# Kernel optimization log

Measured on AMD Instinct MI355X. Metric: run time of the kernel, lower is better.

Reference implementation:

```python
import jax, jax.numpy as jnp
import numpy as np

V, A, N, C = 3, 4, 50000, 128


def setup_inputs() -> dict:
    key = jax.random.key(0)
    k1, k2, k3 = jax.random.split(key, 3)
    x = jax.random.normal(k1, (V, A, N, C), dtype=jnp.float32)
    # per-view Linear(in=C, out=C): weight [out,in], bias [out]
    W = jax.random.normal(k2, (V, C, C), dtype=jnp.float32) / np.sqrt(C)
    b = jax.random.normal(k3, (V, C), dtype=jnp.float32) * 0.01
    return {"x": x, "W": W, "b": b}


def reference(x, W, b):
    # per-view linear: out[v,a,n,d] = x[v,a,n,c] @ W[v,d,c]^T + b[v,d]
    out = jnp.einsum('vanc,vdc->vand', x, W) + b[:, None, None, :]
    # view summary: mean over nodes -> [V, A, C]
    s = x.mean(axis=2)
    # attention scores: s . out per node -> [V, A, N]
    scores = jnp.einsum('vac,vanc->van', s, out)
    # tanh then softmax across views (dim 0)
    w = jax.nn.softmax(jnp.tanh(scores), axis=0)
    # weighted combine of views -> [A, N, C]
    return jnp.einsum('van,vanc->anc', w, x)
```

## Files before the change

### kernel.cpp

```cpp
#include <hip/hip_runtime.h>
#include <hip/hip_bf16.h>

#define V 3
#define A 4
#define NN 50000
#define C 128
#define C4 32
#define CHUNKS 128
#define ROWS_PER ((NN + CHUNKS - 1) / CHUNKS)
#define VA (V * A)

__device__ __forceinline__ float dot4(float4 a, float4 b) {
    return a.x * b.x + a.y * b.y + a.z * b.z + a.w * b.w;
}

__device__ __forceinline__ float fast_tanh(float x) {
    float ax = fminf(fabsf(x), 15.f);
    float e  = __expf(2.f * ax);
    float r  = (e - 1.f) * __frcp_rn(e + 1.f);
    return copysignf(r, x);
}

__global__ void k_colsum(const float* __restrict__ x, float* __restrict__ part) {
    const int va    = blockIdx.y;
    const int chunk = blockIdx.x;
    const int n0 = chunk * ROWS_PER;
    const int n1 = (n0 + ROWS_PER < NN) ? (n0 + ROWS_PER) : NN;

    const int lane4 = threadIdx.x & 31;
    const int rowIn = threadIdx.x >> 5;

    const float4* xp = (const float4*)(x + (size_t)va * NN * C);
    float4 acc = {0.f, 0.f, 0.f, 0.f};
    for (int n = n0 + rowIn; n < n1; n += 8) {
        float4 v = xp[(size_t)n * C4 + lane4];
        acc.x += v.x; acc.y += v.y; acc.z += v.z; acc.w += v.w;
    }

    __shared__ float4 red[256];
    red[threadIdx.x] = acc;
    __syncthreads();
    if (threadIdx.x < 32) {
        float4 t = red[threadIdx.x];
        #pragma unroll
        for (int r = 1; r < 8; r++) {
            float4 o = red[threadIdx.x + 32 * r];
            t.x += o.x; t.y += o.y; t.z += o.z; t.w += o.w;
        }
        ((float4*)part)[((size_t)chunk * VA + va) * C4 + lane4] = t;
    }
}

__global__ void k_tvec(const float* __restrict__ part, const float* __restrict__ W,
                       const float* __restrict__ b, float* __restrict__ t,
                       float* __restrict__ c0) {
    const int va = blockIdx.x;
    const int v  = va / A;
    const int c  = threadIdx.x;

    float acc = 0.f;
    #pragma unroll 4
    for (int ch = 0; ch < CHUNKS; ch++)
        acc += part[((size_t)ch * VA + va) * C + c];

    __shared__ float sb[C];
    __shared__ float pb[C];
    sb[c] = acc * (1.0f / (float)NN);
    __syncthreads();

    const float* Wv = W + (size_t)v * C * C;
    float t_acc = 0.f;
    #pragma unroll 8
    for (int d = 0; d < C; d++) t_acc += sb[d] * Wv[d * C + c];
    t[va * C + c] = t_acc;

    pb[c] = sb[c] * b[v * C + c];
    __syncthreads();
    #pragma unroll
    for (int s = 64; s > 0; s >>= 1) {
        if (c < s) pb[c] += pb[c + s];
        __syncthreads();
    }
    if (c == 0) c0[va] = pb[0];
}

__global__ void k_main(const float* __restrict__ x, const float* __restrict__ t,
                       const float* __restrict__ c0, float* __restrict__ out) {
    const int lane = threadIdx.x & 31;
    const int grp  = threadIdx.x >> 5;
    const int a    = blockIdx.y;
    const int n0   = blockIdx.x * 16 + grp * 2;

    const size_t vstride = (size_t)A * NN * C4;
    const float4* xp = (const float4*)x;
    const size_t baseA = ((size_t)a * NN + n0) * C4 + lane;
    const size_t baseB = baseA + C4;

    float4 xa0 = xp[baseA];
    float4 xa1 = xp[baseA + vstride];
    float4 xa2 = xp[baseA + 2 * vstride];
    float4 xb0 = xp[baseB];
    float4 xb1 = xp[baseB + vstride];
    float4 xb2 = xp[baseB + 2 * vstride];

    const float4* tp = (const float4*)t;
    float4 t0 = tp[(0 * A + a) * C4 + lane];
    float4 t1 = tp[(1 * A + a) * C4 + lane];
    float4 t2 = tp[(2 * A + a) * C4 + lane];

    float da0 = dot4(xa0, t0), da1 = dot4(xa1, t1), da2 = dot4(xa2, t2);
    float db0 = dot4(xb0, t0), db1 = dot4(xb1, t1), db2 = dot4(xb2, t2);

    #pragma unroll
    for (int off = 16; off > 0; off >>= 1) {
        da0 += __shfl_xor(da0, off, 32);
        da1 += __shfl_xor(da1, off, 32);
        da2 += __shfl_xor(da2, off, 32);
        db0 += __shfl_xor(db0, off, 32);
        db1 += __shfl_xor(db1, off, 32);
        db2 += __shfl_xor(db2, off, 32);
    }

    const float cc0 = c0[0 * A + a], cc1 = c0[1 * A + a], cc2 = c0[2 * A + a];

    float sa0 = fast_tanh(da0 + cc0);
    float sa1 = fast_tanh(da1 + cc1);
    float sa2 = fast_tanh(da2 + cc2);
    float ma  = fmaxf(sa0, fmaxf(sa1, sa2));
    float ea0 = __expf(sa0 - ma), ea1 = __expf(sa1 - ma), ea2 = __expf(sa2 - ma);
    float inva = __frcp_rn(ea0 + ea1 + ea2);
    float wa0 = ea0 * inva, wa1 = ea1 * inva, wa2 = ea2 * inva;

    float sb0 = fast_tanh(db0 + cc0);
    float sb1 = fast_tanh(db1 + cc1);
    float sb2 = fast_tanh(db2 + cc2);
    float mb  = fmaxf(sb0, fmaxf(sb1, sb2));
    float eb0 = __expf(sb0 - mb), eb1 = __expf(sb1 - mb), eb2 = __expf(sb2 - mb);
    float invb = __frcp_rn(eb0 + eb1 + eb2);
    float wb0 = eb0 * invb, wb1 = eb1 * invb, wb2 = eb2 * invb;

    float4 oa, ob;
    oa.x = wa0 * xa0.x + wa1 * xa1.x + wa2 * xa2.x;
    oa.y = wa0 * xa0.y + wa1 * xa1.y + wa2 * xa2.y;
    oa.z = wa0 * xa0.z + wa1 * xa1.z + wa2 * xa2.z;
    oa.w = wa0 * xa0.w + wa1 * xa1.w + wa2 * xa2.w;
    ob.x = wb0 * xb0.x + wb1 * xb1.x + wb2 * xb2.x;
    ob.y = wb0 * xb0.y + wb1 * xb1.y + wb2 * xb2.y;
    ob.z = wb0 * xb0.z + wb1 * xb1.z + wb2 * xb2.z;
    ob.w = wb0 * xb0.w + wb1 * xb1.w + wb2 * xb2.w;

    float4* op = (float4*)out;
    const size_t obase = ((size_t)a * NN + n0) * C4 + lane;
    op[obase]      = oa;
    op[obase + C4] = ob;
}

extern "C" void kernel_launch(void* const* d_in, const int* in_sizes, int n_in,
                              void* d_out, int out_size, void* d_ws, size_t ws_size,
                              hipStream_t stream) {
    const float* x = (const float*)d_in[0];
    const float* W = (const float*)d_in[1];
    const float* b = (const float*)d_in[2];
    float* out = (float*)d_out;

    float* part = (float*)d_ws;
    float* t    = part + (size_t)CHUNKS * VA * C;
    float* c0   = t + VA * C;

    k_colsum<<<dim3(CHUNKS, VA), 256, 0, stream>>>(x, part);
    k_tvec<<<VA, C, 0, stream>>>(part, W, b, t, c0);
    k_main<<<dim3(NN / 16, A), 256, 0, stream>>>(x, t, c0, out);
}
```

Measured before the change: 506.0 us.

## Reverse main-pass row order, use nontemporal stores, split tvec reduction, unroll colsum

The main kernel now walks rows in reverse, so the rows the column-sum pass touched last are read first and may still sit in the large last-level cache. Output stores become nontemporal so they do not evict x from cache. k_tvec now runs 256 threads, with each half reducing half of the chunks and half of the W rows, then combining the halves through shared memory. The colsum loop gains an unroll pragma. The reverse order only pays off if a meaningful part of x stays cached between the two kernels, and the extra syncs in tvec are a minor cost.

```diff
diff --git a/kernel.cpp b/kernel.cpp
--- a/kernel.cpp
+++ b/kernel.cpp
@@ -9,6 +9,8 @@
 #define CHUNKS 128
 #define ROWS_PER ((NN + CHUNKS - 1) / CHUNKS)
 #define VA (V * A)
+
+typedef float nf4 __attribute__((ext_vector_type(4)));
 
 __device__ __forceinline__ float dot4(float4 a, float4 b) {
     return a.x * b.x + a.y * b.y + a.z * b.z + a.w * b.w;
@@ -32,6 +34,7 @@
 
     const float4* xp = (const float4*)(x + (size_t)va * NN * C);
     float4 acc = {0.f, 0.f, 0.f, 0.f};
+    #pragma unroll 4
     for (int n = n0 + rowIn; n < n1; n += 8) {
         float4 v = xp[(size_t)n * C4 + lane4];
         acc.x += v.x; acc.y += v.y; acc.z += v.z; acc.w += v.w;
@@ -54,34 +57,43 @@
 __global__ void k_tvec(const float* __restrict__ part, const float* __restrict__ W,
                        const float* __restrict__ b, float* __restrict__ t,
                        float* __restrict__ c0) {
-    const int va = blockIdx.x;
-    const int v  = va / A;
-    const int c  = threadIdx.x;
+    const int va   = blockIdx.x;
+    const int v    = va / A;
+    const int c    = threadIdx.x & 127;
+    const int half = threadIdx.x >> 7;
 
     float acc = 0.f;
-    #pragma unroll 4
-    for (int ch = 0; ch < CHUNKS; ch++)
+    #pragma unroll 8
+    for (int ch = half * 64; ch < half * 64 + 64; ch++)
         acc += part[((size_t)ch * VA + va) * C + c];
 
+    __shared__ float red[2][C];
     __shared__ float sb[C];
     __shared__ float pb[C];
-    sb[c] = acc * (1.0f / (float)NN);
+    red[half][c] = acc;
+    __syncthreads();
+    if (threadIdx.x < C)
+        sb[c] = (red[0][c] + red[1][c]) * (1.0f / (float)NN);
     __syncthreads();
 
     const float* Wv = W + (size_t)v * C * C;
     float t_acc = 0.f;
     #pragma unroll 8
-    for (int d = 0; d < C; d++) t_acc += sb[d] * Wv[d * C + c];
-    t[va * C + c] = t_acc;
-
-    pb[c] = sb[c] * b[v * C + c];
+    for (int d = half * 64; d < half * 64 + 64; d++)
+        t_acc += sb[d] * Wv[d * C + c];
+    red[half][c] = t_acc;
+    __syncthreads();
+    if (threadIdx.x < C) {
+        t[va * C + c] = red[0][c] + red[1][c];
+        pb[c] = sb[c] * b[v * C + c];
+    }
     __syncthreads();
     #pragma unroll
     for (int s = 64; s > 0; s >>= 1) {
-        if (c < s) pb[c] += pb[c + s];
+        if (threadIdx.x < s) pb[threadIdx.x] += pb[threadIdx.x + s];
         __syncthreads();
     }
-    if (c == 0) c0[va] = pb[0];
+    if (threadIdx.x == 0) c0[va] = pb[0];
 }
 
 __global__ void k_main(const float* __restrict__ x, const float* __restrict__ t,
@@ -89,7 +101,7 @@
     const int lane = threadIdx.x & 31;
     const int grp  = threadIdx.x >> 5;
     const int a    = blockIdx.y;
-    const int n0   = blockIdx.x * 16 + grp * 2;
+    const int n0   = (NN - 16) - blockIdx.x * 16 + grp * 2;
 
     const size_t vstride = (size_t)A * NN * C4;
     const float4* xp = (const float4*)x;
@@ -139,7 +151,7 @@
     float invb = __frcp_rn(eb0 + eb1 + eb2);
     float wb0 = eb0 * invb, wb1 = eb1 * invb, wb2 = eb2 * invb;
 
-    float4 oa, ob;
+    nf4 oa, ob;
     oa.x = wa0 * xa0.x + wa1 * xa1.x + wa2 * xa2.x;
     oa.y = wa0 * xa0.y + wa1 * xa1.y + wa2 * xa2.y;
     oa.z = wa0 * xa0.z + wa1 * xa1.z + wa2 * xa2.z;
@@ -149,10 +161,10 @@
     ob.z = wb0 * xb0.z + wb1 * xb1.z + wb2 * xb2.z;
     ob.w = wb0 * xb0.w + wb1 * xb1.w + wb2 * xb2.w;
 
-    float4* op = (float4*)out;
+    nf4* op = (nf4*)out;
     const size_t obase = ((size_t)a * NN + n0) * C4 + lane;
-    op[obase]      = oa;
-    op[obase + C4] = ob;
+    __builtin_nontemporal_store(oa, op + obase);
+    __builtin_nontemporal_store(ob, op + obase + C4);
 }
 
 extern "C" void kernel_launch(void* const* d_in, const int* in_sizes, int n_in,
@@ -168,6 +180,6 @@
     float* c0   = t + VA * C;
 
     k_colsum<<<dim3(CHUNKS, VA), 256, 0, stream>>>(x, part);
-    k_tvec<<<VA, C, 0, stream>>>(part, W, b, t, c0);
+    k_tvec<<<VA, 256, 0, stream>>>(part, W, b, t, c0);
     k_main<<<dim3(NN / 16, A), 256, 0, stream>>>(x, t, c0, out);
 }
```

Result: faster. 489.8 us (-3.2%).
